# Kernel tuning notes

Hardware: AMD Instinct MI355X
Metric: run time of the kernel (lower is better)

## Reference

```python
import jax, jax.numpy as jnp
import numpy as np
import math

B, C, H, W = 2, 256, 64, 64
E = 256           # embed_dim
AE = 64           # angle embed dim = embed_dim // 4
NH = 3            # num angle hypotheses
HEADS = 8
HALF = AE // 2    # 32 sin/cos frequencies

# 3x3 kernel tap grid (dy, dx), row-major, matching torchvision DeformConv2d tap order
KY = jnp.array([-1,-1,-1, 0,0,0, 1,1,1], jnp.float32)
KX = jnp.array([-1, 0, 1,-1,0,1,-1,0,1], jnp.float32)
# assumed angle hypothesis deltas around the predicted angle
HYPO_DELTAS = (-math.pi/12, 0.0, math.pi/12)


def conv2d(x, w, b, pad):
    y = jax.lax.conv_general_dilated(x, w, (1, 1), [(pad, pad), (pad, pad)],
                                     dimension_numbers=('NCHW', 'OIHW', 'NCHW'))
    return y + b[None, :, None, None]


def gen_offsets(angles):
    """Rotate the base 3x3 kernel taps by the per-pixel angle; offset = rotated - base.
    angles: (B, H*W, 1) -> offsets (B, 18, H, W), (dy,dx) interleaved per tap."""
    a = angles.reshape(-1, H, W)
    c = jnp.cos(a)[..., None]           # (B,H,W,1)
    s = jnp.sin(a)[..., None]
    ry = KX * s + KY * c                # rotated y of each tap, (B,H,W,9)
    rx = KX * c - KY * s                # rotated x
    off = jnp.stack([ry - KY, rx - KX], axis=-1)   # (B,H,W,9,2)
    return off.reshape(-1, H, W, 18).transpose(0, 3, 1, 2)


def deform_conv(x, offsets, w, b):
    """DeformConv2d k=3, stride=1, pad=1, dilation=1, zero padding outside.
    x (B,C,H,W), offsets (B,18,H,W), w (O,C,3,3)."""
    off = offsets.reshape(x.shape[0], 9, 2, H, W)
    oy = off[:, :, 0].transpose(0, 2, 3, 1)          # (B,H,W,9)
    ox = off[:, :, 1].transpose(0, 2, 3, 1)
    hh = jnp.arange(H, dtype=jnp.float32)[None, :, None, None]
    ww = jnp.arange(W, dtype=jnp.float32)[None, None, :, None]
    py = hh + KY + oy                                # sample y, (B,H,W,9)
    px = ww + KX + ox
    y0 = jnp.floor(py)
    x0 = jnp.floor(px)
    wy = (py - y0)[:, None]                          # (B,1,H,W,9)
    wx = (px - x0)[:, None]

    def gather(yi, xi):
        valid = (yi >= 0) & (yi <= H - 1) & (xi >= 0) & (xi <= W - 1)
        yc = jnp.clip(yi, 0, H - 1).astype(jnp.int32)
        xc = jnp.clip(xi, 0, W - 1).astype(jnp.int32)
        g = jax.vmap(lambda img, yy, xx: img[:, yy, xx])(x, yc, xc)  # (B,C,H,W,9)
        return g * valid[:, None].astype(x.dtype)

    samp = (gather(y0, x0) * (1 - wy) * (1 - wx)
            + gather(y0, x0 + 1) * (1 - wy) * wx
            + gather(y0 + 1, x0) * wy * (1 - wx)
            + gather(y0 + 1, x0 + 1) * wy * wx)      # (B,C,H,W,9)
    w9 = w.reshape(w.shape[0], w.shape[1], 9)
    return jnp.einsum('bchwk,ock->bohw', samp, w9) + b[None, :, None, None]


def angle_encode(angles, freq_mult, w1, b1, ln_g, ln_b, w2, b2):
    an = (angles / (math.pi / 2))[..., 0]                       # (B,HW) le90 norm
    dim_t = jnp.arange(HALF, dtype=jnp.float32) / HALF * math.pi
    ae = an[..., None] * (freq_mult * dim_t)                    # (B,HW,HALF)
    emb = jnp.concatenate([jnp.sin(ae), jnp.cos(ae)], axis=-1)  # (B,HW,AE)
    h = emb @ w1.T + b1
    mu = h.mean(-1, keepdims=True)
    var = h.var(-1, keepdims=True)
    h = (h - mu) * jax.lax.rsqrt(var + 1e-5) * ln_g + ln_b
    return jax.nn.relu(h) @ w2.T + b2


def mha(q, kv, in_w, in_b, out_w, out_b):
    # q (L,1,E), kv (L,NH,E); torch nn.MultiheadAttention math
    wq, wk, wv = jnp.split(in_w, 3, axis=0)
    bq, bk, bv = jnp.split(in_b, 3)
    hd = E // HEADS
    Q = (q @ wq.T + bq).reshape(-1, 1, HEADS, hd).transpose(0, 2, 1, 3)
    K = (kv @ wk.T + bk).reshape(-1, NH, HEADS, hd).transpose(0, 2, 1, 3)
    V = (kv @ wv.T + bv).reshape(-1, NH, HEADS, hd).transpose(0, 2, 1, 3)
    attn = jax.nn.softmax(jnp.einsum('lhqd,lhkd->lhqk', Q, K) / math.sqrt(hd), axis=-1)
    o = jnp.einsum('lhqk,lhkd->lhqd', attn, V).transpose(0, 2, 1, 3).reshape(-1, 1, E)
    return o @ out_w.T + out_b


def group_norm(x, g, b, groups=32, eps=1e-5):
    Bq, Cc, Hh, Ww = x.shape
    xg = x.reshape(Bq, groups, Cc // groups, Hh, Ww)
    mu = xg.mean((2, 3, 4), keepdims=True)
    var = xg.var((2, 3, 4), keepdims=True)
    xn = ((xg - mu) * jax.lax.rsqrt(var + eps)).reshape(x.shape)
    return xn * g[None, :, None, None] + b[None, :, None, None]


def setup_inputs() -> dict:
    key = jax.random.key(0)
    ks = iter(jax.random.split(key, 32))
    r = lambda *s: jax.random.normal(next(ks), s, jnp.float32) * 0.05
    z = lambda *s: jnp.zeros(s, jnp.float32)
    return {
        'features': jax.random.normal(next(ks), (B, C, H, W), jnp.float32),
        'ap_w1': r(C // 4, C, 3, 3), 'ap_b1': z(C // 4),
        'ap_w2': r(1, C // 4, 1, 1), 'ap_b2': z(1),
        'freq_mult': jnp.ones((HALF,), jnp.float32),
        'ae_w1': r(AE, AE), 'ae_b1': z(AE),
        'ae_ln_g': jnp.ones((AE,), jnp.float32), 'ae_ln_b': z(AE),
        'ae_w2': r(AE, AE), 'ae_b2': z(AE),
        'dc_w': r(E, C, 3, 3), 'dc_b': z(E),
        'attn_in_w': r(3 * E, E), 'attn_in_b': z(3 * E),
        'attn_out_w': r(E, E), 'attn_out_b': z(E),
        'ja_w1': r(E, E + AE, 1, 1), 'ja_b1': z(E),
        'ja_w2': r(E, E, 1, 1), 'ja_b2': z(E),
        'op_w1': r(E, E, 3, 3), 'op_b1': z(E),
        'gn_g': jnp.ones((E,), jnp.float32), 'gn_b': z(E),
        'op_w2': r(E, E, 1, 1), 'op_b2': z(E),
    }


def reference(features, ap_w1, ap_b1, ap_w2, ap_b2, freq_mult, ae_w1, ae_b1,
              ae_ln_g, ae_ln_b, ae_w2, ae_b2, dc_w, dc_b, attn_in_w, attn_in_b,
              attn_out_w, attn_out_b, ja_w1, ja_b1, ja_w2, ja_b2, op_w1, op_b1,
              gn_g, gn_b, op_w2, op_b2):
    # 1) angle prediction
    h1 = jax.nn.relu(conv2d(features, ap_w1, ap_b1, 1))
    angles = conv2d(h1, ap_w2, ap_b2, 0).reshape(B, H * W, 1)
    # 2) periodic angle encoding
    angle_embed = angle_encode(angles, freq_mult, ae_w1, ae_b1, ae_ln_g, ae_ln_b, ae_w2, ae_b2)
    # 3) rotation-aware deformable alignment
    aligned = deform_conv(features, gen_offsets(angles), dc_w, dc_b)
    # 4) multi-angle hypotheses fused by per-pixel attention
    cand = [deform_conv(features, gen_offsets(angles + d), dc_w, dc_b) for d in HYPO_DELTAS]
    feat_stack = jnp.stack(cand, axis=1)                       # (B,NH,E,H,W)
    q = aligned.transpose(0, 2, 3, 1).reshape(B * H * W, 1, E)
    kv = feat_stack.transpose(0, 3, 4, 1, 2).reshape(B * H * W, NH, E)
    fused = mha(q, kv, attn_in_w, attn_in_b, attn_out_w, attn_out_b)
    fused = fused.reshape(B, H, W, E).transpose(0, 3, 1, 2)
    # 5) joint angle-spatial attention gate
    ae_sp = angle_embed.reshape(B, H, W, AE).transpose(0, 3, 1, 2)
    ji = jnp.concatenate([fused, ae_sp], axis=1)
    gate = jax.nn.sigmoid(conv2d(jax.nn.relu(conv2d(ji, ja_w1, ja_b1, 0)), ja_w2, ja_b2, 0))
    enh = fused * gate + fused
    # 6) output projection
    o = jax.nn.relu(group_norm(conv2d(enh, op_w1, op_b1, 1), gn_g, gn_b))
    return conv2d(o, op_w2, op_b2, 0)
```

## Files before the change

kernel.cpp:

```cpp
#include <hip/hip_runtime.h>

#define PI_F 3.14159265358979323846f
#define HWSZ 4096
#define NPIX 8192

typedef __attribute__((ext_vector_type(8))) short short8;
typedef __attribute__((ext_vector_type(4))) short short4_t;
typedef __attribute__((ext_vector_type(4))) float f32x4;

__device__ __forceinline__ short f2bf(float x){
  unsigned u = __float_as_uint(x);
  unsigned r = (u + 0x7FFFu + ((u >> 16) & 1u)) >> 16;
  return (short)r;
}
__device__ __forceinline__ float bf2f(short v){
  return __uint_as_float(((unsigned)(unsigned short)v) << 16);
}

__device__ __forceinline__ float wsum64(float v){
  #pragma unroll
  for (int m = 32; m >= 1; m >>= 1) v += __shfl_xor(v, m, 64);
  return v;
}
__device__ __forceinline__ float wsum8(float v){
  v += __shfl_xor(v, 1, 64);
  v += __shfl_xor(v, 2, 64);
  v += __shfl_xor(v, 4, 64);
  return v;
}

__device__ __forceinline__ void gl_lds(const short* g, short* s){
  __builtin_amdgcn_global_load_lds(
      (const __attribute__((address_space(1))) unsigned int*)g,
      (__attribute__((address_space(3))) unsigned int*)s, 16, 0, 0);
}

__global__ void k_prep(const float* __restrict__ dc_w, const float* __restrict__ op_w1,
    const float* __restrict__ ap_w1,
    const float* __restrict__ s0, const float* __restrict__ s1,
    const float* __restrict__ s2, const float* __restrict__ s3, const float* __restrict__ s4,
    short* __restrict__ enh_pad, short* __restrict__ Bdc, short* __restrict__ B2op,
    short* __restrict__ B3, short* __restrict__ d0, short* __restrict__ d1,
    short* __restrict__ d2, short* __restrict__ d3, short* __restrict__ d4){
  __shared__ short tile[2304];
  int bx = blockIdx.x, tid = threadIdx.x;
  if (bx < 2178){
    int i = bx*256 + tid;
    if (i < 557568) ((short4_t*)enh_pad)[i] = (short4_t){0,0,0,0};
  } else if (bx < 2434){
    int o = bx - 2178;
    const float* wo = dc_w + (size_t)o*2304;
    for (int i = tid; i < 2304; i += 256){
      int c = i / 9, k = i - c*9;
      tile[k*256 + c] = f2bf(wo[i]);
    }
    __syncthreads();
    for (int i = tid; i < 2304; i += 256){
      int k = i >> 8, c = i & 255;
      Bdc[((size_t)(k*256 + o))*256 + c] = tile[i];
    }
  } else if (bx < 2690){
    int o = bx - 2434;
    const float* wo = op_w1 + (size_t)o*2304;
    for (int i = tid; i < 2304; i += 256){
      int c = i / 9, k = i - c*9;
      tile[k*256 + c] = f2bf(wo[i]);
    }
    __syncthreads();
    short* out = B2op + (size_t)o*2304;
    for (int i = tid; i < 2304; i += 256) out[i] = tile[i];
  } else if (bx < 3330){
    int n = bx - 2690, c = tid;
    short hi = 0;
    if (n < 576){
      int o = n & 63, k = n >> 6;
      hi = f2bf(ap_w1[((size_t)o*256 + c)*9 + k]);
    }
    B3[(size_t)n*512 + c] = hi;
    B3[(size_t)n*512 + 256 + c] = hi;
  } else {
    int i = (bx - 3330)*256 + tid;
    if (i < 196608) d0[i] = f2bf(s0[i]);
    else if (i < 262144) d1[i-196608] = f2bf(s1[i-196608]);
    else if (i < 344064) d2[i-262144] = f2bf(s2[i-262144]);
    else if (i < 409600) d3[i-344064] = f2bf(s3[i-344064]);
    else if (i < 475136) d4[i-409600] = f2bf(s4[i-409600]);
  }
}

__global__ void k_nchw_split(const float* __restrict__ in, short* __restrict__ feat_bf,
    short* __restrict__ A3){
  __shared__ float tile[32][33];
  int b = blockIdx.z;
  int p0 = blockIdx.x * 32, c0 = blockIdx.y * 32;
  int tx = threadIdx.x, ty = threadIdx.y;
  #pragma unroll
  for (int i = ty; i < 32; i += 8)
    tile[i][tx] = in[((size_t)b*256 + c0 + i)*HWSZ + p0 + tx];
  __syncthreads();
  #pragma unroll
  for (int i = ty; i < 32; i += 8){
    float x = tile[tx][i];
    short hi = f2bf(x);
    short lo = f2bf(x - bf2f(hi));
    size_t p = (size_t)b*HWSZ + p0 + i;
    feat_bf[p*256 + c0 + tx] = hi;
    A3[p*512 + c0 + tx] = hi;
    A3[p*512 + 256 + c0 + tx] = lo;
  }
}

template<int EPI, int BM, int BN = 128>
__global__ __launch_bounds__(256) void k_gemml(const short* __restrict__ A,
    const short* __restrict__ B, void* __restrict__ Cv,
    const float* __restrict__ bias, const short* __restrict__ aux,
    int K, int ldc){
  constexpr int NWC = BN/64;
  constexpr int NWR = 4/NWC;
  constexpr int WM = BM/NWR;
  constexpr int AF = WM/16;
  __shared__ alignas(16) short sA[2][BM*32];
  __shared__ alignas(16) short sB[2][BN*32];
  int tid = threadIdx.x;
  int w = tid >> 6, l = tid & 63;
  int wc = w % NWC, wr = w / NWC;
  int ml = l & 15, g = l >> 4;
  int srow = tid >> 2;
  int sch = (tid & 3)*8;
  int m0 = blockIdx.x*BM, n0 = blockIdx.y*BN;
  const short* Agp = A + (size_t)(m0 + srow)*K + sch;
  const short* Bgp = B + (size_t)(n0 + srow)*K + sch;
  short* sAd = &sA[0][srow*32 + sch];
  short* sBd = &sB[0][srow*32 + sch];
  f32x4 acc[AF][4];
  #pragma unroll
  for (int i = 0; i < AF; ++i)
    #pragma unroll
    for (int j = 0; j < 4; ++j) acc[i][j] = (f32x4){0.f,0.f,0.f,0.f};

  #define STAGE(bf, kt) { \
    _Pragma("unroll") \
    for (int c = 0; c < BM/64; ++c) \
      gl_lds(Agp + (size_t)(c*64)*K + (kt)*32, sAd + (bf)*BM*32 + c*2048); \
    _Pragma("unroll") \
    for (int c = 0; c < BN/64; ++c) \
      gl_lds(Bgp + (size_t)(c*64)*K + (kt)*32, sBd + (bf)*BN*32 + c*2048); \
  }
  int nk = K >> 5;
  STAGE(0, 0)
  int buf = 0;
  for (int kt = 0; kt < nk; ++kt){
    __syncthreads();
    if (kt + 1 < nk){ STAGE(buf^1, kt+1) }
    short8 af[AF], bq[4];
    #pragma unroll
    for (int i = 0; i < AF; ++i)
      af[i] = *(const short8*)&sA[buf][(wr*WM + i*16 + ml)*32 + g*8];
    #pragma unroll
    for (int j = 0; j < 4; ++j)
      bq[j] = *(const short8*)&sB[buf][(wc*64 + j*16 + ml)*32 + g*8];
    #pragma unroll
    for (int i = 0; i < AF; ++i)
      #pragma unroll
      for (int j = 0; j < 4; ++j)
        acc[i][j] = __builtin_amdgcn_mfma_f32_16x16x32_bf16(af[i], bq[j], acc[i][j], 0, 0, 0);
    buf ^= 1;
  }
  #undef STAGE

  int m0w = m0 + wr*WM;
  int n0w = n0 + wc*64;
  if constexpr (EPI == 4){
    __shared__ float cst[BM][129];
    #pragma unroll
    for (int fm = 0; fm < AF; ++fm)
      #pragma unroll
      for (int fn = 0; fn < 4; ++fn)
        #pragma unroll
        for (int r = 0; r < 4; ++r){
          int cl = wc*64 + fn*16 + ml;
          cst[wr*WM + fm*16 + g*4 + r][cl] = acc[fm][fn][r] + bias[blockIdx.y*128 + cl];
        }
    __syncthreads();
    int px0 = blockIdx.x*BM;
    int b = px0 >> 12, hw0 = px0 & 4095;
    int o = tid >> 1, seg = (tid & 1)*(BM/2);
    float* op = (float*)Cv + (((size_t)(b*256 + blockIdx.y*128 + o)) << 12) + hw0 + seg;
    #pragma unroll
    for (int i = 0; i < BM/2; i += 4){
      float4 vv = {cst[seg+i][o], cst[seg+i+1][o], cst[seg+i+2][o], cst[seg+i+3][o]};
      *(float4*)(op + i) = vv;
    }
  } else {
    #pragma unroll
    for (int fm = 0; fm < AF; ++fm)
      #pragma unroll
      for (int fn = 0; fn < 4; ++fn)
        #pragma unroll
        for (int r = 0; r < 4; ++r){
          int row = m0w + fm*16 + g*4 + r;
          int col = n0w + fn*16 + ml;
          float v = acc[fm][fn][r];
          if constexpr (EPI == 0){
            ((short*)Cv)[(size_t)row*ldc + col] = f2bf(v);
          } else if constexpr (EPI == 1){
            ((short*)Cv)[(size_t)row*ldc + col] = f2bf(v + bias[col]);
          } else if constexpr (EPI == 2){
            ((short*)Cv)[(size_t)row*ldc + col] = f2bf(fmaxf(v + bias[col], 0.f));
          } else if constexpr (EPI == 3){
            float f = bf2f(aux[(size_t)row*320 + col]);
            float s = 1.f/(1.f + __expf(-(v + bias[col])));
            ((short*)Cv)[(size_t)row*ldc + col] = f2bf(f * (1.f + s));
          } else if constexpr (EPI == 6){
            float f = bf2f(aux[(size_t)row*320 + col]);
            float s = 1.f/(1.f + __expf(-(v + bias[col])));
            int b = row >> 12, hw = row & 4095;
            int pi = b*4356 + ((hw>>6)+1)*66 + (hw&63) + 1;
            ((short*)Cv)[(size_t)pi*256 + col] = f2bf(f * (1.f + s));
          } else if constexpr (EPI == 7){
            ((short*)Cv)[(size_t)(col>>8)*2097152 + (size_t)row*256 + (col&255)] = f2bf(v);
          } else {
            ((float*)Cv)[(size_t)row*ldc + col] = v;
          }
        }
  }
}

__global__ __launch_bounds__(256) void k_igconv(const short* __restrict__ Xpad,
    const short* __restrict__ B2, float* __restrict__ PG){
  __shared__ alignas(16) short sA[2][64*32];
  __shared__ alignas(16) short sB[2][128*32];
  int zg = blockIdx.z;
  int tid = threadIdx.x;
  int w = tid >> 6, l = tid & 63;
  int wr = w & 1, wc = w >> 1;
  int ml = l & 15, g = l >> 4;
  int srow = tid >> 2;
  int sch = (tid & 3)*8;
  int m0 = blockIdx.x*64, n0 = blockIdx.y*128;
  int b = blockIdx.x >> 6, imgrow = blockIdx.x & 63;
  int qbase = b*4356 + (imgrow+1)*66 + srow + 1;
  const short* Bgp = B2 + (size_t)(n0 + srow)*2304 + zg*768 + sch;
  short* sAd = &sA[0][srow*32 + sch];
  short* sBd = &sB[0][srow*32 + sch];
  int toff[3];
  #pragma unroll
  for (int i = 0; i < 3; ++i){
    int t = zg*3 + i;
    toff[i] = (t/3 - 1)*66 + (t%3) - 1;
  }
  f32x4 acc[2][4];
  #pragma unroll
  for (int i = 0; i < 2; ++i)
    #pragma unroll
    for (int j = 0; j < 4; ++j) acc[i][j] = (f32x4){0.f,0.f,0.f,0.f};

  #define STG(bf, kt) { \
    int tap = (kt) >> 3, cofs = ((kt) & 7)*32; \
    gl_lds(Xpad + (size_t)(qbase + toff[tap])*256 + cofs + sch, sAd + (bf)*2048); \
    gl_lds(Bgp + (kt)*32, sBd + (bf)*4096); \
    gl_lds(Bgp + (size_t)64*2304 + (kt)*32, sBd + (bf)*4096 + 2048); \
  }
  STG(0, 0)
  int buf = 0;
  for (int kt = 0; kt < 24; ++kt){
    __syncthreads();
    if (kt < 23){ STG(buf^1, kt+1) }
    short8 af[2], bq[4];
    #pragma unroll
    for (int i = 0; i < 2; ++i)
      af[i] = *(const short8*)&sA[buf][(wr*32 + i*16 + ml)*32 + g*8];
    #pragma unroll
    for (int j = 0; j < 4; ++j)
      bq[j] = *(const short8*)&sB[buf][(wc*64 + j*16 + ml)*32 + g*8];
    #pragma unroll
    for (int i = 0; i < 2; ++i)
      #pragma unroll
      for (int j = 0; j < 4; ++j)
        acc[i][j] = __builtin_amdgcn_mfma_f32_16x16x32_bf16(af[i], bq[j], acc[i][j], 0, 0, 0);
    buf ^= 1;
  }
  #undef STG

  float* out = PG + (size_t)zg*2097152;
  int m0w = m0 + wr*32;
  int n0w = n0 + wc*64;
  #pragma unroll
  for (int fm = 0; fm < 2; ++fm)
    #pragma unroll
    for (int fn = 0; fn < 4; ++fn)
      #pragma unroll
      for (int r = 0; r < 4; ++r){
        int row = m0w + fm*16 + g*4 + r;
        int col = n0w + fn*16 + ml;
        out[(size_t)row*256 + col] = acc[fm][fn][r];
      }
}

__global__ void k_aph1enc(const float* __restrict__ T, const float* __restrict__ b1,
    const float* __restrict__ w2, const float* __restrict__ b2,
    const float* __restrict__ freq,
    const float* __restrict__ ew1, const float* __restrict__ eb1,
    const float* __restrict__ lng, const float* __restrict__ lnb,
    const float* __restrict__ ew2, const float* __restrict__ eb2,
    short* __restrict__ gateA, int2* __restrict__ moff, float4* __restrict__ mw){
  const int KYi[9] = {-1,-1,-1,0,0,0,1,1,1};
  const int KXi[9] = {-1,0,1,-1,0,1,-1,0,1};
  __shared__ float sang[4];
  int lane = threadIdx.x & 63;
  int wid = threadIdx.x >> 6;
  int p = blockIdx.x*4 + wid;
  int hw = p & 4095;
  int h = hw >> 6, w = hw & 63;
  float acc = b1[lane];
  #pragma unroll
  for (int k = 0; k < 9; ++k){
    int y = h + KYi[k], x = w + KXi[k];
    if (y < 0 || y > 63 || x < 0 || x > 63) continue;
    acc += T[(size_t)(p + KYi[k]*64 + KXi[k])*640 + k*64 + lane];
  }
  float av = wsum64(fmaxf(acc, 0.f) * w2[lane]) + b2[0];
  if (lane == 0) sang[wid] = av;
  float an = av * (2.0f / PI_F);
  int f = lane & 31;
  float ph = an * freq[f] * ((float)f * (PI_F / 32.0f));
  float emb = (lane < 32) ? __sinf(ph) : __cosf(ph);
  float hh = eb1[lane];
  const float* w1r = ew1 + lane*64;
  #pragma unroll 8
  for (int i = 0; i < 64; ++i){
    float e = __shfl(emb, i, 64);
    hh = fmaf(e, w1r[i], hh);
  }
  float mu = wsum64(hh) * (1.0f/64.0f);
  float d = hh - mu;
  float var = wsum64(d*d) * (1.0f/64.0f);
  float hn = fmaf(d * rsqrtf(var + 1e-5f), lng[lane], lnb[lane]);
  float r = fmaxf(hn, 0.f);
  float o = eb2[lane];
  const float* w2r = ew2 + lane*64;
  #pragma unroll 8
  for (int i = 0; i < 64; ++i){
    float e = __shfl(r, i, 64);
    o = fmaf(e, w2r[i], o);
  }
  gateA[(size_t)p*320 + 256 + lane] = f2bf(o);
  __syncthreads();
  int tid = threadIdx.x;
  if (tid < 108){
    int lp = tid / 27;
    int j = tid - lp*27;
    int pp = blockIdx.x*4 + lp;
    int hyp = j / 9;
    int tap = j - hyp*9;
    float ky = (float)(tap/3 - 1), kx = (float)(tap - (tap/3)*3 - 1);
    float a = sang[lp] + ((float)hyp - 1.0f) * (PI_F / 12.0f);
    float sn = __sinf(a), cs = __cosf(a);
    int b2i = pp >> 12, hw2 = pp & 4095;
    float py = (float)(hw2 >> 6) + kx*sn + ky*cs;
    float px = (float)(hw2 & 63) + kx*cs - ky*sn;
    float y0f = floorf(py), x0f = floorf(px);
    float wy = py - y0f, wx = px - x0f;
    int y0 = (int)y0f, x0 = (int)x0f;
    bool vx0 = (unsigned)x0 < 64u, vx1 = (unsigned)(x0+1) < 64u;
    bool vy0 = (unsigned)y0 < 64u, vy1 = (unsigned)(y0+1) < 64u;
    int xb = vx0 ? x0 : (vx1 ? x0+1 : 0);
    float sx0 = vx0 ? 1.f-wx : (vx1 ? wx : 0.f);
    float sx1 = (vx0 && vx1) ? wx : 0.f;
    int ry0 = vy0 ? y0 : 0;
    int ry1 = vy1 ? y0+1 : 0;
    float vw0 = vy0 ? 1.f-wy : 0.f;
    float vw1 = vy1 ? wy : 0.f;
    int base = (b2i << 12);
    int mi = pp*27 + j;
    moff[mi] = make_int2(tap*4194304 + (base + ry0*64 + xb)*512,
                         tap*4194304 + (base + ry1*64 + xb)*512);
    mw[mi] = make_float4(vw0*sx0, vw0*sx1, vw1*sx0, vw1*sx1);
  }
}

__global__ __launch_bounds__(256, 4) void k_sample(const short* __restrict__ G,
    const int2* __restrict__ moff, const float4* __restrict__ mw,
    const float* __restrict__ bias, short* __restrict__ cand){
  __shared__ int2 smo[216];
  __shared__ float4 smw[216];
  int id = blockIdx.x;
  int sw = (id & 7)*128 + (id >> 3);
  int tid = threadIdx.x;
  int pbase = sw*8;
  if (tid < 216){
    smo[tid] = moff[pbase*27 + tid];
    smw[tid] = mw[pbase*27 + tid];
  }
  __syncthreads();
  int lp = (tid >> 6)*2 + ((tid >> 5) & 1);
  int p = pbase + lp;
  int c8 = (tid & 31)*8;
  float av[3][8];
  {
    float4 b0 = *(const float4*)(bias + c8);
    float4 b1 = *(const float4*)(bias + c8 + 4);
    #pragma unroll
    for (int h2 = 0; h2 < 3; ++h2){
      av[h2][0]=b0.x; av[h2][1]=b0.y; av[h2][2]=b0.z; av[h2][3]=b0.w;
      av[h2][4]=b1.x; av[h2][5]=b1.y; av[h2][6]=b1.z; av[h2][7]=b1.w;
    }
  }
  #pragma unroll
  for (int hyp = 0; hyp < 3; ++hyp){
    #pragma unroll 3
    for (int tap = 0; tap < 9; ++tap){
      int idx = lp*27 + hyp*9 + tap;
      int2 o = smo[idx];
      float4 wv = smw[idx];
      const short* r0 = (const short*)((const char*)G + o.x) + c8;
      const short* r1 = (const short*)((const char*)G + o.y) + c8;
      short8 v00 = *(const short8*)r0;
      short8 v01 = *(const short8*)(r0 + 256);
      short8 v10 = *(const short8*)r1;
      short8 v11 = *(const short8*)(r1 + 256);
      #pragma unroll
      for (int e = 0; e < 8; ++e){
        float s = wv.x*bf2f(v00[e]) + wv.y*bf2f(v01[e]);
        s += wv.z*bf2f(v10[e]) + wv.w*bf2f(v11[e]);
        av[hyp][e] += s;
      }
    }
  }
  #pragma unroll
  for (int hyp = 0; hyp < 3; ++hyp){
    short8 o;
    #pragma unroll
    for (int e = 0; e < 8; ++e) o[e] = f2bf(av[hyp][e]);
    *(short8*)(cand + ((size_t)hyp*NPIX + p)*256 + c8) = o;
  }
}

__global__ void k_attn(const short* __restrict__ Q, const short* __restrict__ KV,
    short* __restrict__ O){
  int lane = threadIdx.x & 63;
  int p = blockIdx.x*4 + (threadIdx.x >> 6);
  float q[4];
  { short4_t t = *(const short4_t*)(Q + (size_t)p*256 + lane*4);
    #pragma unroll
    for (int j = 0; j < 4; ++j) q[j] = bf2f(t[j]); }
  float kv[3][2][4];
  #pragma unroll
  for (int i = 0; i < 3; ++i){
    const short* rp = KV + (size_t)(i*NPIX + p)*512 + lane*4;
    short4_t kt = *(const short4_t*)rp;
    short4_t vt = *(const short4_t*)(rp + 256);
    #pragma unroll
    for (int j = 0; j < 4; ++j){ kv[i][0][j] = bf2f(kt[j]); kv[i][1][j] = bf2f(vt[j]); }
  }
  const float sc = 0.17677669529663688f;
  float s[3];
  #pragma unroll
  for (int i = 0; i < 3; ++i){
    float d = 0.f;
    #pragma unroll
    for (int j = 0; j < 4; ++j) d = fmaf(q[j], kv[i][0][j], d);
    s[i] = wsum8(d) * sc;
  }
  float m = fmaxf(s[0], fmaxf(s[1], s[2]));
  float e0 = __expf(s[0]-m), e1 = __expf(s[1]-m), e2 = __expf(s[2]-m);
  float inv = 1.f/(e0+e1+e2);
  short4_t ot;
  #pragma unroll
  for (int j = 0; j < 4; ++j)
    ot[j] = f2bf((e0*kv[0][1][j] + e1*kv[1][1][j] + e2*kv[2][1][j]) * inv);
  *(short4_t*)(O + (size_t)p*256 + lane*4) = ot;
}

__global__ void k_sum3stat(const float* __restrict__ PG, const float* __restrict__ bias,
    float* __restrict__ t, float* __restrict__ spart){
  int p0 = blockIdx.x * 8;
  int c = threadIdx.x;
  float bb = bias[c];
  float s = 0.f, s2 = 0.f;
  #pragma unroll
  for (int pp = 0; pp < 8; ++pp){
    size_t idx = (size_t)(p0+pp)*256 + c;
    float v = PG[idx] + PG[idx + 2097152] + PG[idx + 4194304] + bb;
    t[idx] = v;
    s += v; s2 = fmaf(v, v, s2);
  }
  s  += __shfl_xor(s, 1, 64);  s  += __shfl_xor(s, 2, 64);  s  += __shfl_xor(s, 4, 64);
  s2 += __shfl_xor(s2, 1, 64); s2 += __shfl_xor(s2, 2, 64); s2 += __shfl_xor(s2, 4, 64);
  if ((c & 7) == 0){
    int b = p0 >> 12;
    int bg = b*32 + (c >> 3);
    int blk = blockIdx.x & 511;
    spart[(size_t)(bg*512 + blk)*2]     = s;
    spart[(size_t)(bg*512 + blk)*2 + 1] = s2;
  }
}

__global__ void k_gnfin(const float* __restrict__ spart, float* __restrict__ stat){
  int bg = blockIdx.x;
  const float* sp = spart + (size_t)bg*1024;
  float s = 0.f, s2 = 0.f;
  for (int i = threadIdx.x; i < 512; i += 256){
    s += sp[i*2]; s2 += sp[i*2+1];
  }
  s = wsum64(s); s2 = wsum64(s2);
  __shared__ float rs[4], rs2[4];
  int wid = threadIdx.x >> 6;
  if ((threadIdx.x & 63) == 0){ rs[wid] = s; rs2[wid] = s2; }
  __syncthreads();
  if (threadIdx.x == 0){
    float S = rs[0]+rs[1]+rs[2]+rs[3];
    float S2 = rs2[0]+rs2[1]+rs2[2]+rs2[3];
    float mean = S * (1.f/32768.f);
    float var = S2 * (1.f/32768.f) - mean*mean;
    stat[bg*2]   = mean;
    stat[bg*2+1] = rsqrtf(var + 1e-5f);
  }
}

__global__ void k_gnrelu(const float* __restrict__ t, const float* __restrict__ stat,
    const float* __restrict__ gng, const float* __restrict__ gnb,
    short* __restrict__ a){
  int p = blockIdx.x*4 + (threadIdx.x >> 6);
  int c4 = (threadIdx.x & 63)*4;
  int b = p >> 12, g = c4 >> 3;
  float mean = stat[(b*32+g)*2], rstd = stat[(b*32+g)*2+1];
  float4 gg = *(const float4*)(gng + c4);
  float4 bb = *(const float4*)(gnb + c4);
  float4 v = *(const float4*)(t + (size_t)p*256 + c4);
  short4_t o;
  o[0] = f2bf(fmaxf((v.x - mean)*rstd*gg.x + bb.x, 0.f));
  o[1] = f2bf(fmaxf((v.y - mean)*rstd*gg.y + bb.y, 0.f));
  o[2] = f2bf(fmaxf((v.z - mean)*rstd*gg.z + bb.z, 0.f));
  o[3] = f2bf(fmaxf((v.w - mean)*rstd*gg.w + bb.w, 0.f));
  *(short4_t*)(a + (size_t)p*256 + c4) = o;
}

extern "C" void kernel_launch(void* const* d_in, const int* in_sizes, int n_in,
                              void* d_out, int out_size, void* d_ws, size_t ws_size,
                              hipStream_t stream){
  (void)in_sizes; (void)n_in; (void)out_size; (void)ws_size;
  const float* features   = (const float*)d_in[0];
  const float* ap_w1      = (const float*)d_in[1];
  const float* ap_b1      = (const float*)d_in[2];
  const float* ap_w2      = (const float*)d_in[3];
  const float* ap_b2      = (const float*)d_in[4];
  const float* freq       = (const float*)d_in[5];
  const float* ae_w1      = (const float*)d_in[6];
  const float* ae_b1      = (const float*)d_in[7];
  const float* ae_ln_g    = (const float*)d_in[8];
  const float* ae_ln_b    = (const float*)d_in[9];
  const float* ae_w2      = (const float*)d_in[10];
  const float* ae_b2      = (const float*)d_in[11];
  const float* dc_w       = (const float*)d_in[12];
  const float* dc_b       = (const float*)d_in[13];
  const float* attn_in_w  = (const float*)d_in[14];
  const float* attn_in_b  = (const float*)d_in[15];
  const float* attn_out_w = (const float*)d_in[16];
  const float* attn_out_b = (const float*)d_in[17];
  const float* ja_w1      = (const float*)d_in[18];
  const float* ja_b1      = (const float*)d_in[19];
  const float* ja_w2      = (const float*)d_in[20];
  const float* ja_b2      = (const float*)d_in[21];
  const float* op_w1      = (const float*)d_in[22];
  const float* op_b1      = (const float*)d_in[23];
  const float* gn_g       = (const float*)d_in[24];
  const float* gn_b       = (const float*)d_in[25];
  const float* op_w2      = (const float*)d_in[26];
  const float* op_b2      = (const float*)d_in[27];

  char* base = (char*)d_ws;
  #define ALLOC(ty, name, elems) ty* name = (ty*)base; base += (size_t)(elems)*sizeof(ty);
  ALLOC(short, feat_bf, 8192*256)
  ALLOC(short, Bdc,     2304*256)
  ALLOC(short, B2op,    256*2304)
  ALLOC(short, B3ap,    640*512)
  ALLOC(short, inw_bf,  768*256)
  ALLOC(short, wot_bf,  256*256)
  ALLOC(short, jw1_bf,  256*320)
  ALLOC(short, jw2_bf,  256*256)
  ALLOC(short, wop2_bf, 256*256)
  ALLOC(short, Gbuf,    24576*768)
  ALLOC(short, gguard,  64)
  ALLOC(short, cand_bf, 3*8192*256)
  ALLOC(short, O_bf,    8192*256)
  ALLOC(short, gateA,   8192*320)
  ALLOC(short, hid_bf,  8192*256)
  ALLOC(short, enh_pad, 2*4356*256)
  ALLOC(float, tbuf,    8192*256)
  ALLOC(float, gstat,   128)
  ALLOC(float, spart,   65536)
  ALLOC(short, a_bf,    8192*256)
  ALLOC(int,   moffb,   2*NPIX*27)
  ALLOC(float, mwb,     4*NPIX*27)
  #undef ALLOC
  (void)gguard;
  short* A3 = cand_bf;
  float* T_ap = (float*)Gbuf;
  short* KVbuf = Gbuf;
  short* Qbuf  = Gbuf + (size_t)24576*512;
  float* PG    = (float*)Gbuf;
  int2*  moff  = (int2*)moffb;
  float4* mwv  = (float4*)mwb;

  dim3 t32(32, 8);
  k_prep<<<5186, 256, 0, stream>>>(dc_w, op_w1, ap_w1,
      attn_in_w, attn_out_w, ja_w1, ja_w2, op_w2,
      enh_pad, Bdc, B2op, B3ap, inw_bf, wot_bf, jw1_bf, jw2_bf, wop2_bf);
  k_nchw_split<<<dim3(128,8,2), t32, 0, stream>>>(features, feat_bf, A3);

  k_gemml<5,64><<<dim3(128,5), 256, 0, stream>>>(A3, B3ap, T_ap, nullptr, nullptr, 512, 640);
  k_aph1enc<<<2048, 256, 0, stream>>>(T_ap, ap_b1, ap_w2, ap_b2, freq,
                                      ae_w1, ae_b1, ae_ln_g, ae_ln_b, ae_w2, ae_b2,
                                      gateA, moff, mwv);
  k_gemml<7,128><<<dim3(64,18), 256, 0, stream>>>(feat_bf, Bdc, Gbuf, nullptr, nullptr, 256, 2304);
  k_sample<<<1024, 256, 0, stream>>>(Gbuf, moff, mwv, dc_b, cand_bf);
  k_gemml<1,128><<<dim3(192,4), 256, 0, stream>>>(cand_bf, inw_bf + (size_t)256*256, KVbuf,
                                                  attn_in_b + 256, nullptr, 256, 512);
  k_gemml<1,64,64><<<dim3(128,4), 256, 0, stream>>>(cand_bf + (size_t)NPIX*256, inw_bf, Qbuf,
                                                    attn_in_b, nullptr, 256, 256);
  k_attn<<<2048, 256, 0, stream>>>(Qbuf, KVbuf, O_bf);
  k_gemml<1,64,64><<<dim3(128,4), 256, 0, stream>>>(O_bf, wot_bf, gateA, attn_out_b, nullptr, 256, 320);
  k_gemml<2,64,64><<<dim3(128,4), 256, 0, stream>>>(gateA, jw1_bf, hid_bf, ja_b1, nullptr, 320, 256);
  k_gemml<6,64,64><<<dim3(128,4), 256, 0, stream>>>(hid_bf, jw2_bf, enh_pad, ja_b2, gateA, 256, 256);
  k_igconv<<<dim3(128,2,3), 256, 0, stream>>>(enh_pad, B2op, PG);
  k_sum3stat<<<1024, 256, 0, stream>>>(PG, op_b1, tbuf, spart);
  k_gnfin<<<64, 256, 0, stream>>>(spart, gstat);
  k_gnrelu<<<2048, 256, 0, stream>>>(tbuf, gstat, gn_g, gn_b, a_bf);
  k_gemml<4,64><<<dim3(128,2), 256, 0, stream>>>(a_bf, wop2_bf, (float*)d_out, op_b2, nullptr, 256, 256);
}
```

Baseline: 197.7 us.

## Fuse prep/transpose, QKV GEMMs, attention+out-proj, and GroupNorm+final projection

Merges the NCHW split into the weight-prep kernel and runs the K/V and Q projections in one launch. It fuses the per-pixel 3-way attention into the output-projection GEMM through an LDS tile, and fuses GroupNorm+ReLU into the final 1x1 projection with an LDS-transposed NCHW store. This removes four launches and the O_bf and a_bf intermediate round trips through global memory. The cost is heavier per-block work: the attention phase in k_attnproj is recomputed for each of the 4 column blocks, and the larger LDS footprint may lower occupancy.

```diff
diff --git a/kernel.cpp b/kernel.cpp
--- a/kernel.cpp
+++ b/kernel.cpp
@@ -35,14 +35,16 @@
       (__attribute__((address_space(3))) unsigned int*)s, 16, 0, 0);
 }
 
-__global__ void k_prep(const float* __restrict__ dc_w, const float* __restrict__ op_w1,
-    const float* __restrict__ ap_w1,
+__global__ void k_prepall(const float* __restrict__ dc_w, const float* __restrict__ op_w1,
+    const float* __restrict__ ap_w1, const float* __restrict__ features,
     const float* __restrict__ s0, const float* __restrict__ s1,
     const float* __restrict__ s2, const float* __restrict__ s3, const float* __restrict__ s4,
     short* __restrict__ enh_pad, short* __restrict__ Bdc, short* __restrict__ B2op,
-    short* __restrict__ B3, short* __restrict__ d0, short* __restrict__ d1,
+    short* __restrict__ B3, short* __restrict__ feat_bf, short* __restrict__ A3,
+    short* __restrict__ d0, short* __restrict__ d1,
     short* __restrict__ d2, short* __restrict__ d3, short* __restrict__ d4){
   __shared__ short tile[2304];
+  __shared__ float ft[32][33];
   int bx = blockIdx.x, tid = threadIdx.x;
   if (bx < 2178){
     int i = bx*256 + tid;
@@ -78,35 +80,33 @@
     }
     B3[(size_t)n*512 + c] = hi;
     B3[(size_t)n*512 + 256 + c] = hi;
-  } else {
+  } else if (bx < 5186){
     int i = (bx - 3330)*256 + tid;
     if (i < 196608) d0[i] = f2bf(s0[i]);
     else if (i < 262144) d1[i-196608] = f2bf(s1[i-196608]);
     else if (i < 344064) d2[i-262144] = f2bf(s2[i-262144]);
     else if (i < 409600) d3[i-344064] = f2bf(s3[i-344064]);
     else if (i < 475136) d4[i-409600] = f2bf(s4[i-409600]);
-  }
-}
-
-__global__ void k_nchw_split(const float* __restrict__ in, short* __restrict__ feat_bf,
-    short* __restrict__ A3){
-  __shared__ float tile[32][33];
-  int b = blockIdx.z;
-  int p0 = blockIdx.x * 32, c0 = blockIdx.y * 32;
-  int tx = threadIdx.x, ty = threadIdx.y;
-  #pragma unroll
-  for (int i = ty; i < 32; i += 8)
-    tile[i][tx] = in[((size_t)b*256 + c0 + i)*HWSZ + p0 + tx];
-  __syncthreads();
-  #pragma unroll
-  for (int i = ty; i < 32; i += 8){
-    float x = tile[tx][i];
-    short hi = f2bf(x);
-    short lo = f2bf(x - bf2f(hi));
-    size_t p = (size_t)b*HWSZ + p0 + i;
-    feat_bf[p*256 + c0 + tx] = hi;
-    A3[p*512 + c0 + tx] = hi;
-    A3[p*512 + 256 + c0 + tx] = lo;
+  } else {
+    int bid = bx - 5186;
+    int z = bid >> 10;
+    int rem = bid & 1023;
+    int p0 = (rem & 127)*32, c0 = (rem >> 7)*32;
+    int tx = tid & 31, ty = tid >> 5;
+    #pragma unroll
+    for (int i = ty; i < 32; i += 8)
+      ft[i][tx] = features[((size_t)z*256 + c0 + i)*HWSZ + p0 + tx];
+    __syncthreads();
+    #pragma unroll
+    for (int i = ty; i < 32; i += 8){
+      float x = ft[tx][i];
+      short hi = f2bf(x);
+      short lo = f2bf(x - bf2f(hi));
+      size_t p = (size_t)z*HWSZ + p0 + i;
+      feat_bf[p*256 + c0 + tx] = hi;
+      A3[p*512 + c0 + tx] = hi;
+      A3[p*512 + 256 + c0 + tx] = lo;
+    }
   }
 }
 
@@ -224,6 +224,152 @@
           }
         }
   }
+}
+
+__global__ __launch_bounds__(256) void k_qkv(const short* __restrict__ cand,
+    const short* __restrict__ inw, const float* __restrict__ inb,
+    short* __restrict__ KV, short* __restrict__ Qb){
+  const short* A; const short* B; short* C; const float* bias; int ldc, m0, n0;
+  if (blockIdx.y < 4){
+    A = cand; B = inw + (size_t)256*256; C = KV; bias = inb + 256; ldc = 512;
+    m0 = blockIdx.x*128; n0 = blockIdx.y*128;
+  } else {
+    if (blockIdx.x >= 128) return;
+    A = cand + (size_t)NPIX*256; B = inw; C = Qb; bias = inb; ldc = 256;
+    m0 = (blockIdx.x >> 1)*128; n0 = (blockIdx.x & 1)*128;
+  }
+  __shared__ alignas(16) short sA[2][128*32];
+  __shared__ alignas(16) short sB[2][128*32];
+  int tid = threadIdx.x;
+  int w = tid >> 6, l = tid & 63;
+  int wc = w & 1, wr = w >> 1;
+  int ml = l & 15, g = l >> 4;
+  int srow = tid >> 2;
+  int sch = (tid & 3)*8;
+  const short* Agp = A + (size_t)(m0 + srow)*256 + sch;
+  const short* Bgp = B + (size_t)(n0 + srow)*256 + sch;
+  short* sAd = &sA[0][srow*32 + sch];
+  short* sBd = &sB[0][srow*32 + sch];
+  f32x4 acc[4][4];
+  #pragma unroll
+  for (int i = 0; i < 4; ++i)
+    #pragma unroll
+    for (int j = 0; j < 4; ++j) acc[i][j] = (f32x4){0.f,0.f,0.f,0.f};
+  #define STG2(bf, kt) { \
+    gl_lds(Agp + (kt)*32, sAd + (bf)*4096); \
+    gl_lds(Agp + (size_t)64*256 + (kt)*32, sAd + (bf)*4096 + 2048); \
+    gl_lds(Bgp + (kt)*32, sBd + (bf)*4096); \
+    gl_lds(Bgp + (size_t)64*256 + (kt)*32, sBd + (bf)*4096 + 2048); \
+  }
+  STG2(0, 0)
+  int buf = 0;
+  for (int kt = 0; kt < 8; ++kt){
+    __syncthreads();
+    if (kt + 1 < 8){ STG2(buf^1, kt+1) }
+    short8 af[4], bq[4];
+    #pragma unroll
+    for (int i = 0; i < 4; ++i)
+      af[i] = *(const short8*)&sA[buf][(wr*64 + i*16 + ml)*32 + g*8];
+    #pragma unroll
+    for (int j = 0; j < 4; ++j)
+      bq[j] = *(const short8*)&sB[buf][(wc*64 + j*16 + ml)*32 + g*8];
+    #pragma unroll
+    for (int i = 0; i < 4; ++i)
+      #pragma unroll
+      for (int j = 0; j < 4; ++j)
+        acc[i][j] = __builtin_amdgcn_mfma_f32_16x16x32_bf16(af[i], bq[j], acc[i][j], 0, 0, 0);
+    buf ^= 1;
+  }
+  #undef STG2
+  int m0w = m0 + wr*64;
+  int n0w = n0 + wc*64;
+  #pragma unroll
+  for (int fm = 0; fm < 4; ++fm)
+    #pragma unroll
+    for (int fn = 0; fn < 4; ++fn)
+      #pragma unroll
+      for (int r = 0; r < 4; ++r){
+        int row = m0w + fm*16 + g*4 + r;
+        int col = n0w + fn*16 + ml;
+        C[(size_t)row*ldc + col] = f2bf(acc[fm][fn][r] + bias[col]);
+      }
+}
+
+__global__ __launch_bounds__(256) void k_attnproj(const short* __restrict__ Qb,
+    const short* __restrict__ KVb, const short* __restrict__ wot,
+    const float* __restrict__ outb, short* __restrict__ gateA){
+  __shared__ alignas(16) short sO[64*256];
+  __shared__ alignas(16) short sB[2][64*32];
+  int tid = threadIdx.x;
+  int m0 = blockIdx.x*64, n0 = blockIdx.y*64;
+  int srow = tid >> 2, sch = (tid & 3)*8;
+  const short* Bgp = wot + (size_t)(n0 + srow)*256 + sch;
+  short* sBd = &sB[0][srow*32 + sch];
+  gl_lds(Bgp, sBd);
+  int lane = tid & 63;
+  int sub = tid >> 6;
+  const float sc = 0.17677669529663688f;
+  #pragma unroll 2
+  for (int it = 0; it < 16; ++it){
+    int lp = it*4 + sub;
+    int p = m0 + lp;
+    float q[4];
+    { short4_t t = *(const short4_t*)(Qb + (size_t)p*256 + lane*4);
+      #pragma unroll
+      for (int j = 0; j < 4; ++j) q[j] = bf2f(t[j]); }
+    float kv[3][2][4];
+    #pragma unroll
+    for (int i = 0; i < 3; ++i){
+      const short* rp = KVb + (size_t)(i*NPIX + p)*512 + lane*4;
+      short4_t kt = *(const short4_t*)rp;
+      short4_t vt = *(const short4_t*)(rp + 256);
+      #pragma unroll
+      for (int j = 0; j < 4; ++j){ kv[i][0][j] = bf2f(kt[j]); kv[i][1][j] = bf2f(vt[j]); }
+    }
+    float s[3];
+    #pragma unroll
+    for (int i = 0; i < 3; ++i){
+      float d = 0.f;
+      #pragma unroll
+      for (int j = 0; j < 4; ++j) d = fmaf(q[j], kv[i][0][j], d);
+      s[i] = wsum8(d) * sc;
+    }
+    float m = fmaxf(s[0], fmaxf(s[1], s[2]));
+    float e0 = __expf(s[0]-m), e1 = __expf(s[1]-m), e2 = __expf(s[2]-m);
+    float inv = 1.f/(e0+e1+e2);
+    short4_t ot;
+    #pragma unroll
+    for (int j = 0; j < 4; ++j)
+      ot[j] = f2bf((e0*kv[0][1][j] + e1*kv[1][1][j] + e2*kv[2][1][j]) * inv);
+    *(short4_t*)&sO[lp*256 + lane*4] = ot;
+  }
+  int w = sub, ml = lane & 15, g = lane >> 4;
+  f32x4 acc[4];
+  #pragma unroll
+  for (int j = 0; j < 4; ++j) acc[j] = (f32x4){0.f,0.f,0.f,0.f};
+  int buf = 0;
+  for (int kt = 0; kt < 8; ++kt){
+    __syncthreads();
+    if (kt + 1 < 8) gl_lds(Bgp + (kt+1)*32, sBd + (buf^1)*2048);
+    short8 af = *(const short8*)&sO[(w*16 + ml)*256 + kt*32 + g*8];
+    short8 bq[4];
+    #pragma unroll
+    for (int j = 0; j < 4; ++j)
+      bq[j] = *(const short8*)&sB[buf][(j*16 + ml)*32 + g*8];
+    #pragma unroll
+    for (int j = 0; j < 4; ++j)
+      acc[j] = __builtin_amdgcn_mfma_f32_16x16x32_bf16(af, bq[j], acc[j], 0, 0, 0);
+    buf ^= 1;
+  }
+  int m0w = m0 + w*16;
+  #pragma unroll
+  for (int fn = 0; fn < 4; ++fn)
+    #pragma unroll
+    for (int r = 0; r < 4; ++r){
+      int row = m0w + g*4 + r;
+      int col = n0 + fn*16 + ml;
+      gateA[(size_t)row*320 + col] = f2bf(acc[fn][r] + outb[col]);
+    }
 }
 
 __global__ __launch_bounds__(256) void k_igconv(const short* __restrict__ Xpad,
@@ -436,42 +582,6 @@
   }
 }
 
-__global__ void k_attn(const short* __restrict__ Q, const short* __restrict__ KV,
-    short* __restrict__ O){
-  int lane = threadIdx.x & 63;
-  int p = blockIdx.x*4 + (threadIdx.x >> 6);
-  float q[4];
-  { short4_t t = *(const short4_t*)(Q + (size_t)p*256 + lane*4);
-    #pragma unroll
-    for (int j = 0; j < 4; ++j) q[j] = bf2f(t[j]); }
-  float kv[3][2][4];
-  #pragma unroll
-  for (int i = 0; i < 3; ++i){
-    const short* rp = KV + (size_t)(i*NPIX + p)*512 + lane*4;
-    short4_t kt = *(const short4_t*)rp;
-    short4_t vt = *(const short4_t*)(rp + 256);
-    #pragma unroll
-    for (int j = 0; j < 4; ++j){ kv[i][0][j] = bf2f(kt[j]); kv[i][1][j] = bf2f(vt[j]); }
-  }
-  const float sc = 0.17677669529663688f;
-  float s[3];
-  #pragma unroll
-  for (int i = 0; i < 3; ++i){
-    float d = 0.f;
-    #pragma unroll
-    for (int j = 0; j < 4; ++j) d = fmaf(q[j], kv[i][0][j], d);
-    s[i] = wsum8(d) * sc;
-  }
-  float m = fmaxf(s[0], fmaxf(s[1], s[2]));
-  float e0 = __expf(s[0]-m), e1 = __expf(s[1]-m), e2 = __expf(s[2]-m);
-  float inv = 1.f/(e0+e1+e2);
-  short4_t ot;
-  #pragma unroll
-  for (int j = 0; j < 4; ++j)
-    ot[j] = f2bf((e0*kv[0][1][j] + e1*kv[1][1][j] + e2*kv[2][1][j]) * inv);
-  *(short4_t*)(O + (size_t)p*256 + lane*4) = ot;
-}
-
 __global__ void k_sum3stat(const float* __restrict__ PG, const float* __restrict__ bias,
     float* __restrict__ t, float* __restrict__ spart){
   int p0 = blockIdx.x * 8;
@@ -518,22 +628,87 @@
   }
 }
 
-__global__ void k_gnrelu(const float* __restrict__ t, const float* __restrict__ stat,
-    const float* __restrict__ gng, const float* __restrict__ gnb,
-    short* __restrict__ a){
-  int p = blockIdx.x*4 + (threadIdx.x >> 6);
-  int c4 = (threadIdx.x & 63)*4;
-  int b = p >> 12, g = c4 >> 3;
-  float mean = stat[(b*32+g)*2], rstd = stat[(b*32+g)*2+1];
-  float4 gg = *(const float4*)(gng + c4);
-  float4 bb = *(const float4*)(gnb + c4);
-  float4 v = *(const float4*)(t + (size_t)p*256 + c4);
-  short4_t o;
-  o[0] = f2bf(fmaxf((v.x - mean)*rstd*gg.x + bb.x, 0.f));
-  o[1] = f2bf(fmaxf((v.y - mean)*rstd*gg.y + bb.y, 0.f));
-  o[2] = f2bf(fmaxf((v.z - mean)*rstd*gg.z + bb.z, 0.f));
-  o[3] = f2bf(fmaxf((v.w - mean)*rstd*gg.w + bb.w, 0.f));
-  *(short4_t*)(a + (size_t)p*256 + c4) = o;
+__global__ __launch_bounds__(256) void k_gnproj(const float* __restrict__ t,
+    const float* __restrict__ stat, const float* __restrict__ gng,
+    const float* __restrict__ gnb, const short* __restrict__ w2,
+    const float* __restrict__ b2, float* __restrict__ out){
+  __shared__ float cst[64*132];
+  __shared__ alignas(16) short sB[2][128*32];
+  short* sA = (short*)cst;
+  int tid = threadIdx.x;
+  int m0 = blockIdx.x*64;
+  int b = m0 >> 12;
+  int srow = tid >> 2, sch = (tid & 3)*8;
+  const short* Bgp = w2 + (size_t)(blockIdx.y*128 + srow)*256 + sch;
+  short* sBd = &sB[0][srow*32 + sch];
+  gl_lds(Bgp, sBd);
+  gl_lds(Bgp + (size_t)64*256, sBd + 2048);
+  #pragma unroll 4
+  for (int it = 0; it < 16; ++it){
+    int c = it*256 + tid;
+    int row = c >> 6;
+    int col = (c & 63)*4;
+    int g4 = col >> 3;
+    float mean = stat[(b*32+g4)*2], rstd = stat[(b*32+g4)*2+1];
+    float4 v = *(const float4*)(t + (size_t)(m0+row)*256 + col);
+    float4 gg = *(const float4*)(gng + col);
+    float4 bbv = *(const float4*)(gnb + col);
+    short4_t o;
+    o[0] = f2bf(fmaxf((v.x - mean)*rstd*gg.x + bbv.x, 0.f));
+    o[1] = f2bf(fmaxf((v.y - mean)*rstd*gg.y + bbv.y, 0.f));
+    o[2] = f2bf(fmaxf((v.z - mean)*rstd*gg.z + bbv.z, 0.f));
+    o[3] = f2bf(fmaxf((v.w - mean)*rstd*gg.w + bbv.w, 0.f));
+    *(short4_t*)&sA[row*256 + col] = o;
+  }
+  int w = tid >> 6, l = tid & 63;
+  int wr = w & 1, wc = w >> 1;
+  int ml = l & 15, g = l >> 4;
+  f32x4 acc[2][4];
+  #pragma unroll
+  for (int i = 0; i < 2; ++i)
+    #pragma unroll
+    for (int j = 0; j < 4; ++j) acc[i][j] = (f32x4){0.f,0.f,0.f,0.f};
+  int buf = 0;
+  for (int kt = 0; kt < 8; ++kt){
+    __syncthreads();
+    if (kt + 1 < 8){
+      gl_lds(Bgp + (kt+1)*32, sBd + (buf^1)*4096);
+      gl_lds(Bgp + (size_t)64*256 + (kt+1)*32, sBd + (buf^1)*4096 + 2048);
+    }
+    short8 af[2], bq[4];
+    #pragma unroll
+    for (int i = 0; i < 2; ++i)
+      af[i] = *(const short8*)&sA[(wr*32 + i*16 + ml)*256 + kt*32 + g*8];
+    #pragma unroll
+    for (int j = 0; j < 4; ++j)
+      bq[j] = *(const short8*)&sB[buf][(wc*64 + j*16 + ml)*32 + g*8];
+    #pragma unroll
+    for (int i = 0; i < 2; ++i)
+      #pragma unroll
+      for (int j = 0; j < 4; ++j)
+        acc[i][j] = __builtin_amdgcn_mfma_f32_16x16x32_bf16(af[i], bq[j], acc[i][j], 0, 0, 0);
+    buf ^= 1;
+  }
+  __syncthreads();
+  #pragma unroll
+  for (int fm = 0; fm < 2; ++fm)
+    #pragma unroll
+    for (int fn = 0; fn < 4; ++fn)
+      #pragma unroll
+      for (int r = 0; r < 4; ++r){
+        int cl = wc*64 + fn*16 + ml;
+        cst[(wr*32 + fm*16 + g*4 + r)*132 + cl] = acc[fm][fn][r] + b2[blockIdx.y*128 + cl];
+      }
+  __syncthreads();
+  int hw0 = m0 & 4095;
+  int o = tid >> 1, seg = (tid & 1)*32;
+  float* op = out + (((size_t)(b*256 + blockIdx.y*128 + o)) << 12) + hw0 + seg;
+  #pragma unroll
+  for (int i = 0; i < 32; i += 4){
+    float4 vv = {cst[(seg+i)*132+o], cst[(seg+i+1)*132+o],
+                 cst[(seg+i+2)*132+o], cst[(seg+i+3)*132+o]};
+    *(float4*)(op + i) = vv;
+  }
 }
 
 extern "C" void kernel_launch(void* const* d_in, const int* in_sizes, int n_in,
@@ -583,14 +758,12 @@
   ALLOC(short, Gbuf,    24576*768)
   ALLOC(short, gguard,  64)
   ALLOC(short, cand_bf, 3*8192*256)
-  ALLOC(short, O_bf,    8192*256)
   ALLOC(short, gateA,   8192*320)
   ALLOC(short, hid_bf,  8192*256)
   ALLOC(short, enh_pad, 2*4356*256)
   ALLOC(float, tbuf,    8192*256)
   ALLOC(float, gstat,   128)
   ALLOC(float, spart,   65536)
-  ALLOC(short, a_bf,    8192*256)
   ALLOC(int,   moffb,   2*NPIX*27)
   ALLOC(float, mwb,     4*NPIX*27)
   #undef ALLOC
@@ -603,11 +776,10 @@
   int2*  moff  = (int2*)moffb;
   float4* mwv  = (float4*)mwb;
 
-  dim3 t32(32, 8);
-  k_prep<<<5186, 256, 0, stream>>>(dc_w, op_w1, ap_w1,
+  k_prepall<<<7234, 256, 0, stream>>>(dc_w, op_w1, ap_w1, features,
       attn_in_w, attn_out_w, ja_w1, ja_w2, op_w2,
-      enh_pad, Bdc, B2op, B3ap, inw_bf, wot_bf, jw1_bf, jw2_bf, wop2_bf);
-  k_nchw_split<<<dim3(128,8,2), t32, 0, stream>>>(features, feat_bf, A3);
+      enh_pad, Bdc, B2op, B3ap, feat_bf, A3,
+      inw_bf, wot_bf, jw1_bf, jw2_bf, wop2_bf);
 
   k_gemml<5,64><<<dim3(128,5), 256, 0, stream>>>(A3, B3ap, T_ap, nullptr, nullptr, 512, 640);
   k_aph1enc<<<2048, 256, 0, stream>>>(T_ap, ap_b1, ap_w2, ap_b2, freq,
@@ -615,17 +787,13 @@
                                       gateA, moff, mwv);
   k_gemml<7,128><<<dim3(64,18), 256, 0, stream>>>(feat_bf, Bdc, Gbuf, nullptr, nullptr, 256, 2304);
   k_sample<<<1024, 256, 0, stream>>>(Gbuf, moff, mwv, dc_b, cand_bf);
-  k_gemml<1,128><<<dim3(192,4), 256, 0, stream>>>(cand_bf, inw_bf + (size_t)256*256, KVbuf,
-                                                  attn_in_b + 256, nullptr, 256, 512);
-  k_gemml<1,64,64><<<dim3(128,4), 256, 0, stream>>>(cand_bf + (size_t)NPIX*256, inw_bf, Qbuf,
-                                                    attn_in_b, nullptr, 256, 256);
-  k_attn<<<2048, 256, 0, stream>>>(Qbuf, KVbuf, O_bf);
-  k_gemml<1,64,64><<<dim3(128,4), 256, 0, stream>>>(O_bf, wot_bf, gateA, attn_out_b, nullptr, 256, 320);
+  k_qkv<<<dim3(192,5), 256, 0, stream>>>(cand_bf, inw_bf, attn_in_b, KVbuf, Qbuf);
+  k_attnproj<<<dim3(128,4), 256, 0, stream>>>(Qbuf, KVbuf, wot_bf, attn_out_b, gateA);
   k_gemml<2,64,64><<<dim3(128,4), 256, 0, stream>>>(gateA, jw1_bf, hid_bf, ja_b1, nullptr, 320, 256);
   k_gemml<6,64,64><<<dim3(128,4), 256, 0, stream>>>(hid_bf, jw2_bf, enh_pad, ja_b2, gateA, 256, 256);
   k_igconv<<<dim3(128,2,3), 256, 0, stream>>>(enh_pad, B2op, PG);
   k_sum3stat<<<1024, 256, 0, stream>>>(PG, op_b1, tbuf, spart);
   k_gnfin<<<64, 256, 0, stream>>>(spart, gstat);
-  k_gnrelu<<<2048, 256, 0, stream>>>(tbuf, gstat, gn_g, gn_b, a_bf);
-  k_gemml<4,64><<<dim3(128,2), 256, 0, stream>>>(a_bf, wop2_bf, (float*)d_out, op_b2, nullptr, 256, 256);
-}
+  k_gnproj<<<dim3(128,2), 256, 0, stream>>>(tbuf, gstat, gn_g, gn_b, wop2_bf, op_b2,
+                                            (float*)d_out);
+}
```

Result: faster. 193.5 us (-2.1%).
